# Optimization experiments

Measured on AMD Instinct MI355X. Metric: run time of the kernel, lower is better.

Reference implementation:

```python
import jax, jax.numpy as jnp
import numpy as np

D = 1024      # d_model
H = 16        # nhead
HD = D // H   # head_dim = 64
R = HD        # rotary_dim (default = head_dim)
N, T = 2, 2048
W_LEFT, W_RIGHT = 127, 128  # attn_window
ROPE_BASE = 10000.0


def _rope(x, cos, sin):
    # x: [N, T, H, HD]; cos/sin: [1, T, 1, R//2]; non-interleaved (rotate-half)
    x1 = x[..., : R // 2]
    x2 = x[..., R // 2 : R]
    rot = jnp.concatenate([x1 * cos - x2 * sin, x2 * cos + x1 * sin], axis=-1)
    if R < x.shape[-1]:
        rot = jnp.concatenate([rot, x[..., R:]], axis=-1)
    return rot


def setup_inputs() -> dict:
    key = jax.random.key(0)
    k1, k2, k3, k4 = jax.random.split(key, 4)
    x = jax.random.normal(k1, (N, T, D), dtype=jnp.float32)
    w_qkv = jax.random.normal(k2, (3 * D, D), dtype=jnp.float32) * 0.02
    w_out = jax.random.normal(k3, (D, D), dtype=jnp.float32) * 0.02
    b_out = jax.random.normal(k4, (D,), dtype=jnp.float32) * 0.02
    return {"x": x, "w_qkv": w_qkv, "w_out": w_out, "b_out": b_out}


def reference(x, w_qkv, w_out, b_out):
    n, t, _ = x.shape
    qkv = (x @ w_qkv.T).reshape(n, t, 3, H, HD)
    q, k, v = qkv[:, :, 0], qkv[:, :, 1], qkv[:, :, 2]  # [N, T, H, HD]

    # Rotary embedding (flash-attn RotaryEmbedding, interleaved=False)
    pos = jnp.arange(t, dtype=jnp.float32)
    inv_freq = 1.0 / (ROPE_BASE ** (jnp.arange(0, R, 2, dtype=jnp.float32) / R))
    freqs = pos[:, None] * inv_freq[None, :]          # [T, R//2]
    cos = jnp.cos(freqs)[None, :, None, :]
    sin = jnp.sin(freqs)[None, :, None, :]
    q = _rope(q, cos, sin)
    k = _rope(k, cos, sin)

    # Sliding-window band mask: keep j in [i - W_LEFT, i + W_RIGHT]
    i = jnp.arange(t)[:, None]
    j = jnp.arange(t)[None, :]
    band = (j >= i - W_LEFT) & (j <= i + W_RIGHT)      # [T, T] bool
    bias = jnp.where(band, 0.0, -jnp.inf).astype(x.dtype)

    scale = np.float32(1.0 / np.sqrt(HD))
    scores = jnp.einsum('nthd,nshd->nhts', q, k) * scale + bias  # [N, H, T, T]
    probs = jax.nn.softmax(scores, axis=-1)
    attn = jnp.einsum('nhts,nshd->nthd', probs, v).reshape(n, t, D)
    return attn @ w_out.T + b_out
```

## Files before the change

kernel.cpp:

```cpp
#include <hip/hip_runtime.h>
#include <math.h>

#define D_MODEL 1024
#define N_HEADS 16
#define HEAD_DIM 64
#define BATCH 2
#define SEQ 2048
#define WIN_L 127
#define WIN_R 128

typedef float f32x4 __attribute__((ext_vector_type(4)));
typedef __bf16 bf16x8 __attribute__((ext_vector_type(8)));
typedef unsigned short ushort8_t __attribute__((ext_vector_type(8)));

typedef const __attribute__((address_space(1))) void* gptr_t;
typedef __attribute__((address_space(3))) void* lptr_t;

__device__ __forceinline__ unsigned short f2bf(float v) {
    unsigned u = __float_as_uint(v);
    unsigned r = (u + 0x7FFF + ((u >> 16) & 1)) >> 16;
    return (unsigned short)r;
}

#define NX_ELEM (4096 * 1024)
#define NW_ELEM (3072 * 1024)
#define NO_ELEM (1024 * 1024)

__global__ __launch_bounds__(256)
void cvt_all(const float* __restrict__ x, const float* __restrict__ wq,
             const float* __restrict__ wo, unsigned short* __restrict__ xb,
             unsigned short* __restrict__ wqb, unsigned short* __restrict__ wob)
{
    int i = (blockIdx.x * 256 + threadIdx.x) * 4;
    const float* src;
    unsigned short* dst;
    int off;
    if (i < NX_ELEM)                 { src = x;  dst = xb;  off = i; }
    else if (i < NX_ELEM + NW_ELEM)  { src = wq; dst = wqb; off = i - NX_ELEM; }
    else                             { src = wo; dst = wob; off = i - NX_ELEM - NW_ELEM; }
    float4 f = *(const float4*)(src + off);
    ushort4 o;
    o.x = f2bf(f.x); o.y = f2bf(f.y); o.z = f2bf(f.z); o.w = f2bf(f.w);
    *(ushort4*)(dst + off) = o;
}

__global__ __launch_bounds__(256, 3)
void gemm_qkv(const unsigned short* __restrict__ A,
              const unsigned short* __restrict__ B,
              unsigned short* __restrict__ qb,
              unsigned short* __restrict__ kb,
              unsigned short* __restrict__ vbT,
              int M, int N, int K)
{
    __shared__ __attribute__((aligned(16))) unsigned short U[17408];
    unsigned short* Al0 = U;
    unsigned short* Bl0 = U + 4096;
    unsigned short* Al1 = U + 8192;
    unsigned short* Bl1 = U + 12288;

    const int tid  = threadIdx.x;
    const int wave = tid >> 6;
    const int lane = tid & 63;
    const int m0 = blockIdx.y * 128;
    const int n0 = blockIdx.x * 128;

    const int wm = (wave >> 1) * 64;
    const int wn = (wave & 1) * 64;
    const int quad = lane >> 4;
    const int l16  = lane & 15;

    const int srow = lane >> 2;
    const int scol = (lane & 3) * 8;

    f32x4 acc[4][4] = {};

    for (int k0 = 0; k0 < K; k0 += 64) {
        __syncthreads();
#pragma unroll
        for (int l = 0; l < 2; ++l) {
            const int r = l * 64 + wave * 16 + srow;
            const unsigned short* gA = A + (size_t)(m0 + r) * K + k0 + scol;
            const unsigned short* gB = B + (size_t)(n0 + r) * K + k0 + scol;
            __builtin_amdgcn_global_load_lds((gptr_t)gA,        (lptr_t)&Al0[r * 32 + scol], 16, 0, 0);
            __builtin_amdgcn_global_load_lds((gptr_t)gB,        (lptr_t)&Bl0[r * 32 + scol], 16, 0, 0);
            __builtin_amdgcn_global_load_lds((gptr_t)(gA + 32), (lptr_t)&Al1[r * 32 + scol], 16, 0, 0);
            __builtin_amdgcn_global_load_lds((gptr_t)(gB + 32), (lptr_t)&Bl1[r * 32 + scol], 16, 0, 0);
        }
        __syncthreads();

#pragma unroll
        for (int kh = 0; kh < 2; ++kh) {
            const unsigned short* Ap = kh ? Al1 : Al0;
            const unsigned short* Bp = kh ? Bl1 : Bl0;
            bf16x8 af[4], bf[4];
#pragma unroll
            for (int i = 0; i < 4; ++i)
                af[i] = *(const bf16x8*)&Ap[(wm + i * 16 + l16) * 32 + quad * 8];
#pragma unroll
            for (int j = 0; j < 4; ++j)
                bf[j] = *(const bf16x8*)&Bp[(wn + j * 16 + l16) * 32 + quad * 8];
#pragma unroll
            for (int i = 0; i < 4; ++i)
#pragma unroll
                for (int j = 0; j < 4; ++j)
                    acc[i][j] = __builtin_amdgcn_mfma_f32_16x16x32_bf16(af[i], bf[j], acc[i][j], 0, 0, 0);
        }
    }

    __syncthreads();

    const int which = (n0 >> 10);
    unsigned short* Tw = U + wave * 4352;

    if (which != 2) {
        float invf[2];
#pragma unroll
        for (int jp = 0; jp < 2; ++jp)
            invf[jp] = exp2f(-(float)(jp * 16 + l16) * 0.41524101186092f);
#pragma unroll
        for (int i = 0; i < 4; ++i) {
            const int tb = (m0 + wm + i * 16 + quad * 4) & 2047;
#pragma unroll
            for (int jp = 0; jp < 2; ++jp)
#pragma unroll
                for (int r = 0; r < 4; ++r) {
                    float s, c;
                    __sincosf((float)(tb + r) * invf[jp], &s, &c);
                    float x1 = acc[i][jp][r], x2 = acc[i][jp + 2][r];
                    acc[i][jp][r]     = x1 * c - x2 * s;
                    acc[i][jp + 2][r] = x2 * c + x1 * s;
                }
        }
#pragma unroll
        for (int i = 0; i < 4; ++i)
#pragma unroll
            for (int j = 0; j < 4; ++j)
#pragma unroll
                for (int r = 0; r < 4; ++r)
                    Tw[(i * 16 + quad * 4 + r) * 68 + j * 16 + l16] = f2bf(acc[i][j][r]);
    } else {
#pragma unroll
        for (int i = 0; i < 4; ++i)
#pragma unroll
            for (int j = 0; j < 4; ++j) {
                ushort4 pv;
                pv.x = f2bf(acc[i][j][0]); pv.y = f2bf(acc[i][j][1]);
                pv.z = f2bf(acc[i][j][2]); pv.w = f2bf(acc[i][j][3]);
                *(ushort4*)&Tw[(j * 16 + l16) * 68 + i * 16 + quad * 4] = pv;
            }
    }

    {
        const int h   = ((n0 + wn) >> 6) & 15;
        const int nb  = (m0 + wm) >> 11;
        const int tw0 = (m0 + wm) & 2047;
        const int lr8 = lane >> 3;
        const int lc8 = (lane & 7) * 8;
        if (which != 2) {
            unsigned short* dst = (which == 0 ? qb : kb);
            unsigned short* gb = dst + (((size_t)nb * 16 + h) * SEQ + tw0) * 64;
#pragma unroll
            for (int c = 0; c < 8; ++c) {
                const int row = c * 8 + lr8;
                ushort4 lo = *(const ushort4*)&Tw[row * 68 + lc8];
                ushort4 hi = *(const ushort4*)&Tw[row * 68 + lc8 + 4];
                ushort8_t v8 = {lo.x, lo.y, lo.z, lo.w, hi.x, hi.y, hi.z, hi.w};
                *(ushort8_t*)&gb[row * 64 + lc8] = v8;
            }
        } else {
            unsigned short* gb = vbT + ((size_t)nb * 16 + h) * 64 * SEQ + tw0;
#pragma unroll
            for (int c = 0; c < 8; ++c) {
                const int drow = c * 8 + lr8;
                ushort4 lo = *(const ushort4*)&Tw[drow * 68 + lc8];
                ushort4 hi = *(const ushort4*)&Tw[drow * 68 + lc8 + 4];
                ushort8_t v8 = {lo.x, lo.y, lo.z, lo.w, hi.x, hi.y, hi.z, hi.w};
                *(ushort8_t*)&gb[(size_t)drow * SEQ + lc8] = v8;
            }
        }
    }
}

__global__ __launch_bounds__(256, 4)
void gemm_out(const unsigned short* __restrict__ A,
              const unsigned short* __restrict__ B,
              const float* __restrict__ bias, float* __restrict__ C,
              int M, int N, int K)
{
    __shared__ __attribute__((aligned(16))) unsigned short Al0[64 * 32];
    __shared__ __attribute__((aligned(16))) unsigned short Al1[64 * 32];
    __shared__ __attribute__((aligned(16))) unsigned short Bl0[128 * 32];
    __shared__ __attribute__((aligned(16))) unsigned short Bl1[128 * 32];

    const int tid  = threadIdx.x;
    const int wave = tid >> 6;
    const int lane = tid & 63;
    const int m0 = blockIdx.y * 64;
    const int n0 = blockIdx.x * 128;

    const int wm = (wave >> 1) * 32;
    const int wn = (wave & 1) * 64;
    const int quad = lane >> 4;
    const int l16  = lane & 15;

    const int srow = lane >> 2;
    const int scol = (lane & 3) * 8;

    f32x4 acc[2][4] = {};

    for (int k0 = 0; k0 < K; k0 += 64) {
        __syncthreads();
        {
            const int r = wave * 16 + srow;
            const unsigned short* gA = A + (size_t)(m0 + r) * K + k0 + scol;
            __builtin_amdgcn_global_load_lds((gptr_t)gA,        (lptr_t)&Al0[r * 32 + scol], 16, 0, 0);
            __builtin_amdgcn_global_load_lds((gptr_t)(gA + 32), (lptr_t)&Al1[r * 32 + scol], 16, 0, 0);
#pragma unroll
            for (int l = 0; l < 2; ++l) {
                const int rb = l * 64 + wave * 16 + srow;
                const unsigned short* gB = B + (size_t)(n0 + rb) * K + k0 + scol;
                __builtin_amdgcn_global_load_lds((gptr_t)gB,        (lptr_t)&Bl0[rb * 32 + scol], 16, 0, 0);
                __builtin_amdgcn_global_load_lds((gptr_t)(gB + 32), (lptr_t)&Bl1[rb * 32 + scol], 16, 0, 0);
            }
        }
        __syncthreads();

#pragma unroll
        for (int kh = 0; kh < 2; ++kh) {
            const unsigned short* Ap = kh ? Al1 : Al0;
            const unsigned short* Bp = kh ? Bl1 : Bl0;
            bf16x8 af[2], bf[4];
#pragma unroll
            for (int i = 0; i < 2; ++i)
                af[i] = *(const bf16x8*)&Ap[(wm + i * 16 + l16) * 32 + quad * 8];
#pragma unroll
            for (int j = 0; j < 4; ++j)
                bf[j] = *(const bf16x8*)&Bp[(wn + j * 16 + l16) * 32 + quad * 8];
#pragma unroll
            for (int i = 0; i < 2; ++i)
#pragma unroll
                for (int j = 0; j < 4; ++j)
                    acc[i][j] = __builtin_amdgcn_mfma_f32_16x16x32_bf16(af[i], bf[j], acc[i][j], 0, 0, 0);
        }
    }

#pragma unroll
    for (int i = 0; i < 2; ++i) {
        const int row_base = m0 + wm + i * 16 + quad * 4;
#pragma unroll
        for (int j = 0; j < 4; ++j) {
            const int col = n0 + wn + j * 16 + l16;
            const float bv = bias[col];
#pragma unroll
            for (int r = 0; r < 4; ++r)
                C[(size_t)(row_base + r) * N + col] = acc[i][j][r] + bv;
        }
    }
}

__global__ __launch_bounds__(256, 3)
void attn_mfma(const unsigned short* __restrict__ qb,
               const unsigned short* __restrict__ kb,
               const unsigned short* __restrict__ vbT,
               unsigned short* __restrict__ attnb)
{
    __shared__ __attribute__((aligned(16))) unsigned short Vl[64 * 328];
    __shared__ __attribute__((aligned(16))) unsigned short Pl[4][2][16 * 40];

    const int tid  = threadIdx.x;
    const int w    = tid >> 6;
    const int lane = tid & 63;
    const int quad = lane >> 4;
    const int l16  = lane & 15;

    const int t0 = blockIdx.x * 64;
    const int h  = blockIdx.y;
    const int nB = blockIdx.z;
    const int nh = nB * 16 + h;

    const int klo_b = max(0, t0 - WIN_L) & ~31;

    {
        const unsigned short* vbase = vbT + (size_t)nh * 64 * SEQ;
#pragma unroll
        for (int k = 0; k < 11; ++k) {
            const int s = k * 256 + tid;
            if (s < 64 * 41) {
                const int row = s / 41;
                const int seg = s - row * 41;
                const int tsrc = min(klo_b + seg * 8, SEQ - 8);
                __builtin_amdgcn_global_load_lds(
                    (gptr_t)(vbase + (size_t)row * SEQ + tsrc),
                    (lptr_t)&Vl[s * 8], 16, 0, 0);
            }
        }
    }
    __syncthreads();

    const int tw  = t0 + w * 16;
    const int klo = max(0, tw - WIN_L) & ~31;
    const int khi = min(SEQ, tw + 16 + WIN_R);
    const int nchunk = (khi - klo + 31) >> 5;

    const unsigned short* qrow = qb + ((size_t)nh * SEQ + tw + l16) * 64;
    bf16x8 aq0 = *(const bf16x8*)(qrow + quad * 8);
    bf16x8 aq1 = *(const bf16x8*)(qrow + 32 + quad * 8);

    const unsigned short* kbase = kb + (size_t)nh * SEQ * 64;

    const int trow = tw + quad * 4;

    f32x4 oacc[4] = {};
    float sm[4] = {0.f, 0.f, 0.f, 0.f};

    bf16x8 kA0, kA1, kB0, kB1;
    {
        const int keyA = klo + 2 * l16;
        const unsigned short* kpA = kbase + (size_t)min(keyA, SEQ - 1) * 64;
        const unsigned short* kpB = kbase + (size_t)min(keyA + 1, SEQ - 1) * 64;
        kA0 = *(const bf16x8*)(kpA + quad * 8);
        kA1 = *(const bf16x8*)(kpA + 32 + quad * 8);
        kB0 = *(const bf16x8*)(kpB + quad * 8);
        kB1 = *(const bf16x8*)(kpB + 32 + quad * 8);
    }

    for (int kc = 0; kc < nchunk; ++kc) {
        const int s0 = klo + kc * 32;
        const int keyA = s0 + 2 * l16;
        const int keyB = keyA + 1;

        bf16x8 nA0 = kA0, nA1 = kA1, nB0 = kB0, nB1 = kB1;
        if (kc + 1 < nchunk) {
            const int kyA = s0 + 32 + 2 * l16;
            const unsigned short* kpA = kbase + (size_t)min(kyA, SEQ - 1) * 64;
            const unsigned short* kpB = kbase + (size_t)min(kyA + 1, SEQ - 1) * 64;
            nA0 = *(const bf16x8*)(kpA + quad * 8);
            nA1 = *(const bf16x8*)(kpA + 32 + quad * 8);
            nB0 = *(const bf16x8*)(kpB + quad * 8);
            nB1 = *(const bf16x8*)(kpB + 32 + quad * 8);
        }

        f32x4 sa = {0.f, 0.f, 0.f, 0.f};
        f32x4 sb = {0.f, 0.f, 0.f, 0.f};
        __builtin_amdgcn_s_setprio(1);
        sa = __builtin_amdgcn_mfma_f32_16x16x32_bf16(aq0, kA0, sa, 0, 0, 0);
        sa = __builtin_amdgcn_mfma_f32_16x16x32_bf16(aq1, kA1, sa, 0, 0, 0);
        sb = __builtin_amdgcn_mfma_f32_16x16x32_bf16(aq0, kB0, sb, 0, 0, 0);
        sb = __builtin_amdgcn_mfma_f32_16x16x32_bf16(aq1, kB1, sb, 0, 0, 0);
        __builtin_amdgcn_s_setprio(0);

        unsigned short* Pc = &Pl[w][kc & 1][0];
#pragma unroll
        for (int r = 0; r < 4; ++r) {
            const int t = trow + r;
            const bool vA = (keyA < khi) && (keyA >= t - WIN_L) && (keyA <= t + WIN_R);
            const bool vB = (keyB < khi) && (keyB >= t - WIN_L) && (keyB <= t + WIN_R);
            float p0 = vA ? exp2f(sa[r] * 0.18033688011f) : 0.f;
            float p1 = vB ? exp2f(sb[r] * 0.18033688011f) : 0.f;
            sm[r] += p0 + p1;
            unsigned pk = (unsigned)f2bf(p0) | ((unsigned)f2bf(p1) << 16);
            *(unsigned*)&Pc[(quad * 4 + r) * 40 + 2 * l16] = pk;
        }

        bf16x8 pf = *(const bf16x8*)&Pc[l16 * 40 + quad * 8];
        const int rel = s0 - klo_b + quad * 8;
        __builtin_amdgcn_s_setprio(1);
#pragma unroll
        for (int j = 0; j < 4; ++j) {
            bf16x8 vf = *(const bf16x8*)&Vl[(j * 16 + l16) * 328 + rel];
            oacc[j] = __builtin_amdgcn_mfma_f32_16x16x32_bf16(pf, vf, oacc[j], 0, 0, 0);
        }
        __builtin_amdgcn_s_setprio(0);

        kA0 = nA0; kA1 = nA1; kB0 = nB0; kB1 = nB1;
    }

#pragma unroll
    for (int r = 0; r < 4; ++r) {
#pragma unroll
        for (int o = 8; o >= 1; o >>= 1) sm[r] += __shfl_xor(sm[r], o, 64);
        sm[r] = 1.0f / sm[r];
    }

#pragma unroll
    for (int j = 0; j < 4; ++j)
#pragma unroll
        for (int r = 0; r < 4; ++r) {
            const int t = trow + r;
            attnb[((size_t)(nB * SEQ + t)) * D_MODEL + h * 64 + j * 16 + l16] =
                f2bf(oacc[j][r] * sm[r]);
        }
}

extern "C" void kernel_launch(void* const* d_in, const int* in_sizes, int n_in,
                              void* d_out, int out_size, void* d_ws, size_t ws_size,
                              hipStream_t stream)
{
    (void)in_sizes; (void)n_in; (void)out_size; (void)ws_size;
    const float* x     = (const float*)d_in[0];
    const float* w_qkv = (const float*)d_in[1];
    const float* w_out = (const float*)d_in[2];
    const float* b_out = (const float*)d_in[3];
    float* out = (float*)d_out;

    const int M = BATCH * SEQ;

    unsigned short* qb  = (unsigned short*)d_ws;
    unsigned short* kb  = qb  + (size_t)4194304;
    unsigned short* vbT = kb  + (size_t)4194304;
    unsigned short* wob = vbT + (size_t)4194304;
    unsigned short* xb  = wob + (size_t)1048576;
    unsigned short* wqb = xb  + (size_t)4194304;
    unsigned short* attnb = xb;

    dim3 blk(256);

    cvt_all<<<dim3((NX_ELEM + NW_ELEM + NO_ELEM) / 4 / 256), blk, 0, stream>>>(
        x, w_qkv, w_out, xb, wqb, wob);

    gemm_qkv<<<dim3(3 * D_MODEL / 128, M / 128), blk, 0, stream>>>(
        xb, wqb, qb, kb, vbT, M, 3 * D_MODEL, D_MODEL);

    attn_mfma<<<dim3(SEQ / 64, N_HEADS, BATCH), blk, 0, stream>>>(qb, kb, vbT, attnb);

    gemm_out<<<dim3(D_MODEL / 128, M / 64), blk, 0, stream>>>(
        attnb, wob, b_out, out, M, D_MODEL, D_MODEL);
}
```

Baseline: 164.3 us.

## Precompute RoPE cos/sin table and load V fragments directly from global

The conversion kernel now also fills a cos/sin table, using accurate cosf/sinf, for every position and frequency pair. The QKV GEMM epilogue reads that table instead of calling __sincosf per element. The attention kernel drops its LDS staging of the V window and the block-wide barrier, and each wave loads its V fragments from global memory inside the key loop. The aim is to remove per-element transcendental work and the LDS fill and sync, at the cost of more scattered global reads. The extra grid for the table appears sized four times too large, so it writes past the table region.

```diff
diff --git a/kernel.cpp b/kernel.cpp
--- a/kernel.cpp
+++ b/kernel.cpp
@@ -25,23 +25,39 @@
 #define NX_ELEM (4096 * 1024)
 #define NW_ELEM (3072 * 1024)
 #define NO_ELEM (1024 * 1024)
+#define NTOT_ELEM (NX_ELEM + NW_ELEM + NO_ELEM)
+#define TAB_ELEM (SEQ * 32)
 
 __global__ __launch_bounds__(256)
 void cvt_all(const float* __restrict__ x, const float* __restrict__ wq,
              const float* __restrict__ wo, unsigned short* __restrict__ xb,
-             unsigned short* __restrict__ wqb, unsigned short* __restrict__ wob)
+             unsigned short* __restrict__ wqb, unsigned short* __restrict__ wob,
+             float2* __restrict__ ctab)
 {
     int i = (blockIdx.x * 256 + threadIdx.x) * 4;
-    const float* src;
-    unsigned short* dst;
-    int off;
-    if (i < NX_ELEM)                 { src = x;  dst = xb;  off = i; }
-    else if (i < NX_ELEM + NW_ELEM)  { src = wq; dst = wqb; off = i - NX_ELEM; }
-    else                             { src = wo; dst = wob; off = i - NX_ELEM - NW_ELEM; }
-    float4 f = *(const float4*)(src + off);
-    ushort4 o;
-    o.x = f2bf(f.x); o.y = f2bf(f.y); o.z = f2bf(f.z); o.w = f2bf(f.w);
-    *(ushort4*)(dst + off) = o;
+    if (i < NTOT_ELEM) {
+        const float* src;
+        unsigned short* dst;
+        int off;
+        if (i < NX_ELEM)                 { src = x;  dst = xb;  off = i; }
+        else if (i < NX_ELEM + NW_ELEM)  { src = wq; dst = wqb; off = i - NX_ELEM; }
+        else                             { src = wo; dst = wob; off = i - NX_ELEM - NW_ELEM; }
+        float4 f = *(const float4*)(src + off);
+        ushort4 o;
+        o.x = f2bf(f.x); o.y = f2bf(f.y); o.z = f2bf(f.z); o.w = f2bf(f.w);
+        *(ushort4*)(dst + off) = o;
+    } else {
+        int e0 = i - NTOT_ELEM;
+#pragma unroll
+        for (int e = 0; e < 4; ++e) {
+            const int idx = e0 + e;
+            const int t = idx >> 5;
+            const int f = idx & 31;
+            const float invf = exp2f(-(float)f * 0.41524101186092f);
+            const float ang = (float)t * invf;
+            ctab[idx] = make_float2(cosf(ang), sinf(ang));
+        }
+    }
 }
 
 __global__ __launch_bounds__(256, 3)
@@ -50,6 +66,7 @@
               unsigned short* __restrict__ qb,
               unsigned short* __restrict__ kb,
               unsigned short* __restrict__ vbT,
+              const float2* __restrict__ ctab,
               int M, int N, int K)
 {
     __shared__ __attribute__((aligned(16))) unsigned short U[17408];
@@ -113,10 +130,6 @@
     unsigned short* Tw = U + wave * 4352;
 
     if (which != 2) {
-        float invf[2];
-#pragma unroll
-        for (int jp = 0; jp < 2; ++jp)
-            invf[jp] = exp2f(-(float)(jp * 16 + l16) * 0.41524101186092f);
 #pragma unroll
         for (int i = 0; i < 4; ++i) {
             const int tb = (m0 + wm + i * 16 + quad * 4) & 2047;
@@ -124,11 +137,10 @@
             for (int jp = 0; jp < 2; ++jp)
 #pragma unroll
                 for (int r = 0; r < 4; ++r) {
-                    float s, c;
-                    __sincosf((float)(tb + r) * invf[jp], &s, &c);
+                    const float2 cs = ctab[(tb + r) * 32 + jp * 16 + l16];
                     float x1 = acc[i][jp][r], x2 = acc[i][jp + 2][r];
-                    acc[i][jp][r]     = x1 * c - x2 * s;
-                    acc[i][jp + 2][r] = x2 * c + x1 * s;
+                    acc[i][jp][r]     = x1 * cs.x - x2 * cs.y;
+                    acc[i][jp + 2][r] = x2 * cs.x + x1 * cs.y;
                 }
         }
 #pragma unroll
@@ -264,7 +276,6 @@
                const unsigned short* __restrict__ vbT,
                unsigned short* __restrict__ attnb)
 {
-    __shared__ __attribute__((aligned(16))) unsigned short Vl[64 * 328];
     __shared__ __attribute__((aligned(16))) unsigned short Pl[4][2][16 * 40];
 
     const int tid  = threadIdx.x;
@@ -278,25 +289,6 @@
     const int nB = blockIdx.z;
     const int nh = nB * 16 + h;
 
-    const int klo_b = max(0, t0 - WIN_L) & ~31;
-
-    {
-        const unsigned short* vbase = vbT + (size_t)nh * 64 * SEQ;
-#pragma unroll
-        for (int k = 0; k < 11; ++k) {
-            const int s = k * 256 + tid;
-            if (s < 64 * 41) {
-                const int row = s / 41;
-                const int seg = s - row * 41;
-                const int tsrc = min(klo_b + seg * 8, SEQ - 8);
-                __builtin_amdgcn_global_load_lds(
-                    (gptr_t)(vbase + (size_t)row * SEQ + tsrc),
-                    (lptr_t)&Vl[s * 8], 16, 0, 0);
-            }
-        }
-    }
-    __syncthreads();
-
     const int tw  = t0 + w * 16;
     const int klo = max(0, tw - WIN_L) & ~31;
     const int khi = min(SEQ, tw + 16 + WIN_R);
@@ -307,6 +299,7 @@
     bf16x8 aq1 = *(const bf16x8*)(qrow + 32 + quad * 8);
 
     const unsigned short* kbase = kb + (size_t)nh * SEQ * 64;
+    const unsigned short* vbase = vbT + (size_t)nh * 64 * SEQ;
 
     const int trow = tw + quad * 4;
 
@@ -329,6 +322,14 @@
         const int keyA = s0 + 2 * l16;
         const int keyB = keyA + 1;
 
+        bf16x8 vf[4];
+        {
+            const int vcol = s0 + quad * 8;
+#pragma unroll
+            for (int j = 0; j < 4; ++j)
+                vf[j] = *(const bf16x8*)(vbase + (size_t)(j * 16 + l16) * SEQ + vcol);
+        }
+
         bf16x8 nA0 = kA0, nA1 = kA1, nB0 = kB0, nB1 = kB1;
         if (kc + 1 < nchunk) {
             const int kyA = s0 + 32 + 2 * l16;
@@ -363,13 +364,10 @@
         }
 
         bf16x8 pf = *(const bf16x8*)&Pc[l16 * 40 + quad * 8];
-        const int rel = s0 - klo_b + quad * 8;
         __builtin_amdgcn_s_setprio(1);
 #pragma unroll
-        for (int j = 0; j < 4; ++j) {
-            bf16x8 vf = *(const bf16x8*)&Vl[(j * 16 + l16) * 328 + rel];
-            oacc[j] = __builtin_amdgcn_mfma_f32_16x16x32_bf16(pf, vf, oacc[j], 0, 0, 0);
-        }
+        for (int j = 0; j < 4; ++j)
+            oacc[j] = __builtin_amdgcn_mfma_f32_16x16x32_bf16(pf, vf[j], oacc[j], 0, 0, 0);
         __builtin_amdgcn_s_setprio(0);
 
         kA0 = nA0; kA1 = nA1; kB0 = nB0; kB1 = nB1;
@@ -411,15 +409,16 @@
     unsigned short* wob = vbT + (size_t)4194304;
     unsigned short* xb  = wob + (size_t)1048576;
     unsigned short* wqb = xb  + (size_t)4194304;
+    float2* ctab = (float2*)(wqb + (size_t)4194304);
     unsigned short* attnb = xb;
 
     dim3 blk(256);
 
-    cvt_all<<<dim3((NX_ELEM + NW_ELEM + NO_ELEM) / 4 / 256), blk, 0, stream>>>(
-        x, w_qkv, w_out, xb, wqb, wob);
+    cvt_all<<<dim3((NTOT_ELEM + TAB_ELEM * 4) / 4 / 256), blk, 0, stream>>>(
+        x, w_qkv, w_out, xb, wqb, wob, ctab);
 
     gemm_qkv<<<dim3(3 * D_MODEL / 128, M / 128), blk, 0, stream>>>(
-        xb, wqb, qb, kb, vbT, M, 3 * D_MODEL, D_MODEL);
+        xb, wqb, qb, kb, vbT, ctab, M, 3 * D_MODEL, D_MODEL);
 
     attn_mfma<<<dim3(SEQ / 64, N_HEADS, BATCH), blk, 0, stream>>>(qb, kb, vbT, attnb);
 
```

Result: slower. 174.4 us (+6.2%).
